# Kernel tuning notes

Measured on AMD Instinct MI355X. Metric: run time of the kernel, lower is better.

Reference implementation:

```python
import jax, jax.numpy as jnp
import numpy as np

EPS_NORM = 1e-5   # o_norm eps
EPS_L2 = 1e-6     # qk l2norm eps
CHUNK = 128       # chunk length for the scan


def _short_conv(x, w):
    # x: [B,T,C], w: [C,K]; causal depthwise conv followed by silu (ShortConvolution)
    K = w.shape[1]
    T = x.shape[1]
    xp = jnp.pad(x, ((0, 0), (K - 1, 0), (0, 0)))
    y = sum(xp[:, i:i + T, :] * w[:, i] for i in range(K))
    return jax.nn.silu(y)


def _l2norm(x):
    return x * jax.lax.rsqrt(jnp.sum(x * x, axis=-1, keepdims=True) + EPS_L2)


def _kda_scan(q, k, v, gk, beta):
    # gated delta rule: S_t = (I - b_t k_t k_t^T) diag(exp(gk_t)) S_{t-1} + b_t k_t v_t^T;  o_t = q_t^T S_t
    # q,k,gk: [B,T,H,Dk]; v: [B,T,H,Dv]; beta: [B,T,H]
    B, T, H, Dk = q.shape
    Dv = v.shape[-1]
    NC = T // CHUNK

    def c4(x):  # [B,T,H,D] -> [NC, CHUNK, B, H, D]
        return jnp.transpose(x.reshape(B, NC, CHUNK, H, x.shape[-1]), (1, 2, 0, 3, 4))

    qc, kc, vc, gc = c4(q), c4(k), c4(v), c4(gk)
    bc = jnp.transpose(beta.reshape(B, NC, CHUNK, H), (1, 2, 0, 3))

    def step(S, inp):  # S: [B,H,Dk,Dv]
        q_t, k_t, v_t, g_t, b_t = inp
        S = S * jnp.exp(g_t)[..., None]                       # per-key-channel decay
        err = v_t - jnp.einsum('bhk,bhkv->bhv', k_t, S)       # delta-rule error
        S = S + b_t[..., None, None] * (k_t[..., None] * err[..., None, :])
        o_t = jnp.einsum('bhk,bhkv->bhv', q_t, S)
        return S, o_t

    @jax.checkpoint
    def chunk_fn(S, xs):
        return jax.lax.scan(step, S, xs)

    S0 = jnp.zeros((B, H, Dk, Dv), q.dtype)
    _, o = jax.lax.scan(chunk_fn, S0, (qc, kc, vc, gc, bc))   # o: [NC, CHUNK, B, H, Dv]
    return jnp.transpose(o.reshape(T, B, H, Dv), (1, 0, 2, 3))


def _forward(hidden_states, q_w, k_w, v_w, q_conv_w, k_conv_w, v_conv_w,
             f_w1, f_w2, b_w, A_log, dt_bias, g_w1, g_w2, g_b2, o_norm_w, o_w):
    B, T, D = hidden_states.shape
    H = A_log.shape[0]
    Dv = o_norm_w.shape[0]
    Dk = q_w.shape[1] // H

    q = _short_conv(hidden_states @ q_w, q_conv_w).reshape(B, T, H, Dk)
    k = _short_conv(hidden_states @ k_w, k_conv_w).reshape(B, T, H, Dk)
    v = _short_conv(hidden_states @ v_w, v_conv_w).reshape(B, T, H, Dv)

    # fused_kda_gate: per-channel log-decay
    g = ((hidden_states @ f_w1) @ f_w2).reshape(B, T, H, Dk)
    gk = -jnp.exp(A_log)[:, None] * jax.nn.softplus(g + dt_bias.reshape(H, Dk))

    beta = jax.nn.sigmoid(hidden_states @ b_w)  # [B,T,H]

    q = _l2norm(q) * (Dk ** -0.5)
    k = _l2norm(k)

    o = _kda_scan(q, k, v, gk, beta)  # [B,T,H,Dv]

    # FusedRMSNormGated(activation='sigmoid')
    gate = ((hidden_states @ g_w1) @ g_w2 + g_b2).reshape(B, T, H, Dv)
    o = o * jax.lax.rsqrt(jnp.mean(o * o, axis=-1, keepdims=True) + EPS_NORM) * o_norm_w
    o = o * jax.nn.sigmoid(gate)

    return o.reshape(B, T, H * Dv) @ o_w


def setup_inputs() -> dict:
    key = jax.random.key(0)
    B, T, D = 2, 4096, 2048
    H, Dk, Dv = 16, 128, 128
    KD, VD = H * Dk, H * Dv
    Kc = 4
    ks = jax.random.split(key, 16)
    s = 0.02
    n = lambda kk, sh: jax.random.normal(kk, sh, jnp.float32) * s
    return dict(
        hidden_states=jax.random.normal(ks[0], (B, T, D), jnp.float32),
        q_w=n(ks[1], (D, KD)), k_w=n(ks[2], (D, KD)), v_w=n(ks[3], (D, VD)),
        q_conv_w=n(ks[4], (KD, Kc)), k_conv_w=n(ks[5], (KD, Kc)), v_conv_w=n(ks[6], (VD, Kc)),
        f_w1=n(ks[7], (D, Dv)), f_w2=n(ks[8], (Dv, KD)),
        b_w=n(ks[9], (D, H)),
        A_log=jnp.log(jax.random.uniform(ks[10], (H,), jnp.float32, 1.0, 16.0)),
        dt_bias=jnp.zeros((KD,), jnp.float32),
        g_w1=n(ks[11], (D, Dv)), g_w2=n(ks[12], (Dv, VD)), g_b2=jnp.zeros((VD,), jnp.float32),
        o_norm_w=jnp.ones((Dv,), jnp.float32),
        o_w=n(ks[13], (VD, D)),
    )


def reference(hidden_states, q_w, k_w, v_w, q_conv_w, k_conv_w, v_conv_w,
              f_w1, f_w2, b_w, A_log, dt_bias, g_w1, g_w2, g_b2, o_norm_w, o_w):
    return _forward(hidden_states, q_w, k_w, v_w, q_conv_w, k_conv_w, v_conv_w,
                    f_w1, f_w2, b_w, A_log, dt_bias, g_w1, g_w2, g_b2, o_norm_w, o_w)
```

## Files before the change

kernel.cpp:

```cpp
#include <hip/hip_runtime.h>
#include <math.h>


constexpr int NB = 2, NT = 4096, ND = 2048, NH = 16, DK = 128, DV = 128;
constexpr int MROWS = NB * NT;
constexpr int BHN   = NB * NH;
constexpr int CCH   = 16;
constexpr int NCH   = NT / CCH;

#define DEV static __device__ __forceinline__

typedef __attribute__((ext_vector_type(8))) short short8;
typedef __attribute__((ext_vector_type(4))) short short4v;
typedef __attribute__((ext_vector_type(4))) float f32x4;

DEV float sigmoidf_(float x) { return 1.0f / (1.0f + expf(-x)); }

DEV float bf2f(unsigned u) { return __uint_as_float(u << 16); }
DEV unsigned f2bf(float f) {
    unsigned u = __float_as_uint(f);
    return (u + 0x7fffu + ((u >> 16) & 1u)) >> 16;
}
DEV unsigned pack2(float a, float b) { return f2bf(a) | (f2bf(b) << 16); }

DEV void gl2lds16(const void* g, void* l) {
    __builtin_amdgcn_global_load_lds(
        (const __attribute__((address_space(1))) unsigned int*)g,
        (__attribute__((address_space(3))) unsigned int*)l, 16, 0, 0);
}
DEV void gl2lds4(const void* g, void* l) {
    __builtin_amdgcn_global_load_lds(
        (const __attribute__((address_space(1))) unsigned int*)g,
        (__attribute__((address_space(3))) unsigned int*)l, 4, 0, 0);
}

template <int CTRL>
DEV float dppadd(float x) {
    int y = __builtin_amdgcn_mov_dpp(__float_as_int(x), CTRL, 0xF, 0xF, true);
    return x + __int_as_float(y);
}
DEV float reduce16f(float x) {
    x = dppadd<0xB1>(x);
    x = dppadd<0x4E>(x);
    x = dppadd<0x141>(x);
    x = dppadd<0x140>(x);
    return x;
}

DEV float4 bflo(uint4 U) {
    return make_float4(bf2f(U.x & 0xffff), bf2f(U.x >> 16),
                       bf2f(U.y & 0xffff), bf2f(U.y >> 16));
}
DEV float4 bfhi(uint4 U) {
    return make_float4(bf2f(U.z & 0xffff), bf2f(U.z >> 16),
                       bf2f(U.w & 0xffff), bf2f(U.w >> 16));
}

DEV short4v lo4(short8 v) { short4v r; r[0]=v[0]; r[1]=v[1]; r[2]=v[2]; r[3]=v[3]; return r; }
DEV short4v hi4(short8 v) { short4v r; r[0]=v[4]; r[1]=v[5]; r[2]=v[6]; r[3]=v[7]; return r; }

DEV f32x4 mfma16(short4v a, short4v b, f32x4 c) {
#if __has_builtin(__builtin_amdgcn_mfma_f32_16x16x16bf16_1k)
    return __builtin_amdgcn_mfma_f32_16x16x16bf16_1k(a, b, c, 0, 0, 0);
#elif __has_builtin(__builtin_amdgcn_mfma_f32_16x16x16_bf16)
    return __builtin_amdgcn_mfma_f32_16x16x16_bf16(a, b, c, 0, 0, 0);
#else
    asm volatile("s_nop 1\n\t"
                 "v_mfma_f32_16x16x16_bf16 %0, %1, %2, %0\n\t"
                 "s_nop 7\n\t"
                 "s_nop 7"
                 : "+v"(c) : "v"(a), "v"(b));
    return c;
#endif
}

template <int OUTBF>
__global__ __launch_bounds__(256) void gemm_bf16(
    const unsigned short* __restrict__ A, const unsigned short* __restrict__ Bt,
    void* __restrict__ Cv, int Md, int Nd, int Kd)
{
    __shared__ unsigned short As[128 * 64];
    __shared__ unsigned short Bs[128 * 64];

    const int nbx = Nd >> 7;
    const int bx = blockIdx.x % nbx;
    const int by = blockIdx.x / nbx;
    const int m0 = by << 7, n0 = bx << 7;
    const int tid = threadIdx.x;
    const int lane = tid & 63, wid = tid >> 6;
    const int wr = wid >> 1, wc = wid & 1;

    const int srow  = tid >> 3;
    const int sslot = (tid & 7) ^ (srow & 7);
    const unsigned short* ag = A  + (size_t)(m0 + srow) * Kd + sslot * 8;
    const unsigned short* bg = Bt + (size_t)(n0 + srow) * Kd + sslot * 8;
    const size_t rstep32 = (size_t)32 * Kd;
    unsigned short* aw = As + wid * 512;
    unsigned short* bw = Bs + wid * 512;

    const int rrow  = lane & 15;
    const int khalf = lane >> 4;
    const int rswz  = rrow & 7;

    f32x4 zf = {0.f, 0.f, 0.f, 0.f};
    f32x4 acc[4][4];
#pragma unroll
    for (int m = 0; m < 4; m++)
#pragma unroll
        for (int n = 0; n < 4; n++) acc[m][n] = zf;

    for (int k0 = 0; k0 < Kd; k0 += 64) {
#pragma unroll
        for (int i = 0; i < 4; i++) {
            gl2lds16(ag + (size_t)i * rstep32 + k0, aw + i * 2048);
            gl2lds16(bg + (size_t)i * rstep32 + k0, bw + i * 2048);
        }
        __syncthreads();
#pragma unroll
        for (int kk = 0; kk < 2; kk++) {
            const int slot = (kk * 4 + khalf) ^ rswz;
            short8 a[4], b[4];
#pragma unroll
            for (int m = 0; m < 4; m++)
                a[m] = *(const short8*)&As[(wr * 64 + m * 16 + rrow) * 64 + slot * 8];
#pragma unroll
            for (int n = 0; n < 4; n++)
                b[n] = *(const short8*)&Bs[(wc * 64 + n * 16 + rrow) * 64 + slot * 8];
#pragma unroll
            for (int m = 0; m < 4; m++)
#pragma unroll
                for (int n = 0; n < 4; n++)
                    acc[m][n] = __builtin_amdgcn_mfma_f32_16x16x32_bf16(
                        a[m], b[n], acc[m][n], 0, 0, 0);
        }
        __syncthreads();
    }

#pragma unroll
    for (int m = 0; m < 4; m++) {
        const int rowb = m0 + wr * 64 + m * 16 + khalf * 4;
#pragma unroll
        for (int n = 0; n < 4; n++) {
            const int col = n0 + wc * 64 + n * 16 + rrow;
#pragma unroll
            for (int r = 0; r < 4; r++) {
                const float v = acc[m][n][r];
                if (OUTBF)
                    ((unsigned short*)Cv)[(size_t)(rowb + r) * Nd + col] =
                        (unsigned short)f2bf(v);
                else
                    ((float*)Cv)[(size_t)(rowb + r) * Nd + col] = v;
            }
        }
    }
}

__global__ __launch_bounds__(256) void wtrans(
    const float* __restrict__ W, unsigned short* __restrict__ Wt, int Kd, int Nd)
{
    __shared__ float T[64][65];
    const int nbk = Kd >> 6;
    const int bk = blockIdx.x % nbk, bn = blockIdx.x / nbk;
    const int k0 = bk << 6, n0 = bn << 6;
    const int tid = threadIdx.x;
    {
        const int r = tid >> 2, cg = tid & 3;
#pragma unroll
        for (int i = 0; i < 4; i++) {
            float4 f = *(const float4*)&W[(size_t)(k0 + r) * Nd + n0 + cg * 16 + i * 4];
            T[r][cg * 16 + i * 4 + 0] = f.x;
            T[r][cg * 16 + i * 4 + 1] = f.y;
            T[r][cg * 16 + i * 4 + 2] = f.z;
            T[r][cg * 16 + i * 4 + 3] = f.w;
        }
    }
    __syncthreads();
    {
        const int n = tid >> 2, kg = tid & 3;
#pragma unroll
        for (int i = 0; i < 2; i++) {
            unsigned o[4];
#pragma unroll
            for (int j = 0; j < 4; j++) {
                const int kk = kg * 16 + i * 8 + 2 * j;
                o[j] = pack2(T[kk][n], T[kk + 1][n]);
            }
            *(uint4*)&Wt[(size_t)(n0 + n) * Kd + k0 + kg * 16 + i * 8] =
                make_uint4(o[0], o[1], o[2], o[3]);
        }
    }
}

__global__ __launch_bounds__(256) void f2bf_k(
    const float* __restrict__ x, unsigned short* __restrict__ y, int n8)
{
    const int i = blockIdx.x * blockDim.x + threadIdx.x;
    if (i < n8) {
        float4 a = *(const float4*)&x[(size_t)i * 8];
        float4 b = *(const float4*)&x[(size_t)i * 8 + 4];
        uint4 o = make_uint4(pack2(a.x, a.y), pack2(a.z, a.w),
                             pack2(b.x, b.y), pack2(b.z, b.w));
        *(uint4*)&y[(size_t)i * 8] = o;
    }
}

template <int MODE>
__global__ __launch_bounds__(256) void conv_silu(
    const unsigned short* __restrict__ pre, const float* __restrict__ cw,
    unsigned short* __restrict__ outp)
{
    const int m = blockIdx.x;
    const int t = m & (NT - 1);
    const int b = m >> 12;
    const int tid = threadIdx.x;
    const int hd = tid * 8;
    const int h  = hd >> 7;
    const int d0 = hd & 127;

    float xr[4][8];
#pragma unroll
    for (int i = 0; i < 4; i++) {
        const int tt = t - 3 + i;
        if (tt >= 0) {
            uint4 u = *(const uint4*)(pre + (size_t)(m - 3 + i) * ND + hd);
            float4 lo = bflo(u), hi = bfhi(u);
            xr[i][0] = lo.x; xr[i][1] = lo.y; xr[i][2] = lo.z; xr[i][3] = lo.w;
            xr[i][4] = hi.x; xr[i][5] = hi.y; xr[i][6] = hi.z; xr[i][7] = hi.w;
        } else {
#pragma unroll
            for (int j = 0; j < 8; j++) xr[i][j] = 0.f;
        }
    }
    float y[8];
    float ssum = 0.f;
#pragma unroll
    for (int j = 0; j < 8; j++) {
        float4 w = *(const float4*)&cw[(size_t)(hd + j) * 4];
        float v = xr[0][j] * w.x + xr[1][j] * w.y + xr[2][j] * w.z + xr[3][j] * w.w;
        v = v * sigmoidf_(v);
        y[j] = v;
        ssum += v * v;
    }
    float scale = 1.f;
    if (MODE >= 1) {
        ssum = reduce16f(ssum);
        scale = rsqrtf(ssum + 1e-6f);
        if (MODE == 2) scale *= 0.08838834764831845f;
    }
    uint4 pk;
    pk.x = pack2(y[0] * scale, y[1] * scale);
    pk.y = pack2(y[2] * scale, y[3] * scale);
    pk.z = pack2(y[4] * scale, y[5] * scale);
    pk.w = pack2(y[6] * scale, y[7] * scale);
    unsigned short* dst = outp + ((size_t)(b * NH + h) * NT + t) * 128 + d0;
    *(uint4*)dst = pk;
}

__global__ __launch_bounds__(256) void gk_k(
    const unsigned short* __restrict__ g, const float* __restrict__ A_log,
    const float* __restrict__ dtb, _Float16* __restrict__ gko)
{
    const int m = blockIdx.x;
    const int t = m & (NT - 1);
    const int b = m >> 12;
    const int tid = threadIdx.x;
    const int hd = tid * 8, h = hd >> 7, d0 = hd & 127;
    const float ea = expf(A_log[h]);
    uint4 u = *(const uint4*)(g + (size_t)m * ND + hd);
    float4 lo = bflo(u), hi = bfhi(u);
    float4 b0 = *(const float4*)&dtb[hd], b1 = *(const float4*)&dtb[hd + 4];
    float xin[8] = {lo.x + b0.x, lo.y + b0.y, lo.z + b0.z, lo.w + b0.w,
                    hi.x + b1.x, hi.y + b1.y, hi.z + b1.z, hi.w + b1.w};
    union { _Float16 h8[8]; uint4 u4; } up;
#pragma unroll
    for (int j = 0; j < 8; j++) {
        float x = xin[j];
        float sp = (x > 20.f) ? x : log1pf(expf(x));
        up.h8[j] = (_Float16)(-ea * sp);
    }
    _Float16* dst = gko + ((size_t)(b * NH + h) * NT + t) * 128 + d0;
    *(uint4*)dst = up.u4;
}

__global__ __launch_bounds__(256) void beta_k(
    const float* __restrict__ hs, const float* __restrict__ bw,
    float* __restrict__ bt)
{
    __shared__ float sh[ND];
    __shared__ float part[16][17];
    const int m = blockIdx.x, tid = threadIdx.x;
    ((float4*)sh)[tid * 2]     = ((const float4*)(hs + (size_t)m * ND))[tid * 2];
    ((float4*)sh)[tid * 2 + 1] = ((const float4*)(hs + (size_t)m * ND))[tid * 2 + 1];
    __syncthreads();
    const int h = tid & 15, seg = tid >> 4;
    float p = 0.f;
#pragma unroll 8
    for (int j = 0; j < 128; j++)
        p += sh[seg * 128 + j] * bw[(size_t)(seg * 128 + j) * 16 + h];
    part[seg][h] = p;
    __syncthreads();
    if (tid < 16) {
        float s = 0.f;
#pragma unroll
        for (int i = 0; i < 16; i++) s += part[i][tid];
        const int t = m & (NT - 1), b = m >> 12;
        bt[(size_t)(b * NH + tid) * NT + t] = sigmoidf_(s);
    }
}

__global__ __launch_bounds__(256) void kda_prep(
    unsigned short* __restrict__ qn, unsigned short* __restrict__ kn,
    unsigned short* __restrict__ vv, unsigned short* __restrict__ gkh,
    const float* __restrict__ bt,
    float* __restrict__ BdB, float* __restrict__ eCB)
{
    __shared__ float cL[16][132];
    __shared__ float kL[16][132];
    __shared__ float qL[16][132];
    __shared__ float kapL[16][132];
    __shared__ float AbL[16][16];
    __shared__ float bL[16];
    __shared__ float sx[16][264];

    const int blk = blockIdx.x;
    const int bh  = blk >> 8;
    const int cc  = blk & 255;
    const int tid = threadIdx.x;
    const size_t ebase  = ((size_t)bh * NT + cc * 16) * 128;
    const size_t chbase = (size_t)bh * NCH + cc;

    if (tid < 16) bL[tid] = bt[(size_t)bh * NT + cc * 16 + tid];

    if (tid < 128) {
        const int d = tid;
        float c = 0.f;
#pragma unroll
        for (int i = 0; i < 16; i++) {
            float g = (float)(((const _Float16*)gkh)[ebase + i * 128 + d]);
            c += g;
            cL[i][d] = c;
            float kv = bf2f(kn[ebase + i * 128 + d]);
            float qv = bf2f(qn[ebase + i * 128 + d]);
            kL[i][d] = kv; qL[i][d] = qv;
            kapL[i][d] = kv * expf(c);
        }
        eCB[chbase * 128 + d] = expf(c);
    }
    __syncthreads();

    if (tid < 128) {
        const int d = tid;
        const int t = d >> 4, rr = d & 15;
        const int sw = (rr & 7) << 3;
        const float clast = cL[15][d];
        unsigned u[8];
#pragma unroll
        for (int e = 0; e < 8; e++) {
            float v0 = bL[2 * e]     * kL[2 * e][d]     * expf(clast - cL[2 * e][d]);
            float v1 = bL[2 * e + 1] * kL[2 * e + 1][d] * expf(clast - cL[2 * e + 1][d]);
            u[e] = pack2(v0, v1);
        }
        const unsigned bs = ((t >> 1) * 16 + rr) * 32 + (t & 1) * 4;
        unsigned short* base = gkh + chbase * 2048;
        *(uint2*)(base + ((bs +  0) ^ sw)) = make_uint2(u[0], u[1]);
        *(uint2*)(base + ((bs +  8) ^ sw)) = make_uint2(u[2], u[3]);
        *(uint2*)(base + ((bs + 16) ^ sw)) = make_uint2(u[4], u[5]);
        *(uint2*)(base + ((bs + 24) ^ sw)) = make_uint2(u[6], u[7]);
    }

    const int si = tid >> 4, sj = tid & 15;
    float aAcc = 0.f, bAcc = 0.f;
    if (si >= sj) {
        for (int d4 = 0; d4 < 128; d4 += 4) {
            float4 ci = *(const float4*)&cL[si][d4];
            float4 cj = *(const float4*)&cL[sj][d4];
            float4 ki = *(const float4*)&kL[si][d4];
            float4 kj = *(const float4*)&kL[sj][d4];
            float4 qi = *(const float4*)&qL[si][d4];
            float w;
            w = expf(ci.x - cj.x); aAcc += ki.x * kj.x * w; bAcc += qi.x * kj.x * w;
            w = expf(ci.y - cj.y); aAcc += ki.y * kj.y * w; bAcc += qi.y * kj.y * w;
            w = expf(ci.z - cj.z); aAcc += ki.z * kj.z * w; bAcc += qi.z * kj.z * w;
            w = expf(ci.w - cj.w); aAcc += ki.w * kj.w * w; bAcc += qi.w * kj.w * w;
        }
    }
    if (si > sj) AbL[si][sj] = aAcc * bL[sj];
    BdB[chbase * 256 + ((si * 16 + sj) ^ ((si & 7) << 2))] = bAcc * bL[sj];
    __syncthreads();

    {
        const int col = tid;
        float x[16];
#pragma unroll
        for (int i = 0; i < 16; i++)
            x[i] = (col < 128) ? kapL[i][col]
                               : bf2f(vv[ebase + (size_t)i * 128 + (col - 128)]);
#pragma unroll
        for (int i = 1; i < 16; i++) {
            float s = x[i];
#pragma unroll
            for (int l = 0; l < 15; l++)
                if (l < i) s -= AbL[i][l] * x[l];
            x[i] = s;
        }
#pragma unroll
        for (int i = 0; i < 16; i++) sx[i][col] = x[i];
    }
    __syncthreads();

    {
        const int row = tid >> 4, q16 = tid & 15;
        const int d0 = q16 * 8;
        const int t  = q16 >> 1;
        const int pos0 = (t >> 1) * 32 + (t & 1) * 4 + (q16 & 1) * 16;
        const int sw = (row & 7) << 3;
        const int oA = pos0 ^ sw;
        const int oB = (pos0 + 8) ^ sw;
        unsigned pu[4], qu[4];
#pragma unroll
        for (int e = 0; e < 4; e++) {
            pu[e] = pack2(-sx[row][d0 + 2 * e], -sx[row][d0 + 2 * e + 1]);
            qu[e] = pack2(qL[row][d0 + 2 * e]     * expf(cL[row][d0 + 2 * e]),
                          qL[row][d0 + 2 * e + 1] * expf(cL[row][d0 + 2 * e + 1]));
        }
        unsigned short* kb = kn + ebase + (size_t)row * 128;
        unsigned short* qb = qn + ebase + (size_t)row * 128;
        *(uint2*)(kb + oA) = make_uint2(pu[0], pu[1]);
        *(uint2*)(kb + oB) = make_uint2(pu[2], pu[3]);
        *(uint2*)(qb + oA) = make_uint2(qu[0], qu[1]);
        *(uint2*)(qb + oB) = make_uint2(qu[2], qu[3]);
    }
    if (tid < 128) {
        const int c = tid;
        unsigned u2[8];
#pragma unroll
        for (int e = 0; e < 8; e++)
            u2[e] = pack2(sx[2 * e][128 + c], sx[2 * e + 1][128 + c]);
        unsigned short* vb = vv + ebase + (size_t)c * 16;
        *(uint4*)(vb)     = make_uint4(u2[0], u2[1], u2[2], u2[3]);
        *(uint4*)(vb + 8) = make_uint4(u2[4], u2[5], u2[6], u2[7]);
    }
}

__global__ __launch_bounds__(64) void kda_scan4(
    const unsigned short* __restrict__ qn, const unsigned short* __restrict__ kn,
    const unsigned short* __restrict__ vv, const unsigned short* __restrict__ khat,
    const float* __restrict__ BdB, const float* __restrict__ eCB,
    float* __restrict__ osc)
{
    __shared__ unsigned short Pl[2][2048];
    __shared__ unsigned short Ql[2][2048];
    __shared__ unsigned short KHl[2][2048];
    __shared__ unsigned short Vl[2][256];
    __shared__ float eCl[2][128];
    __shared__ float Bdl[2][256];

    const int bh = blockIdx.x & 31;
    const int vg = blockIdx.x >> 5;
    const int lane = threadIdx.x;
    const int r16 = lane & 15, h4 = lane >> 4;
    const int bb = bh >> 4, hh = bh & 15;
    const int sw = (r16 & 7) << 3;

    f32x4 Sm[8];
    short4v Shi[8];
    const short4v z4 = {0, 0, 0, 0};
#pragma unroll
    for (int t = 0; t < 8; t++) { Sm[t] = (f32x4){0.f, 0.f, 0.f, 0.f}; Shi[t] = z4; }

    auto issue = [&](int cc, int buf) {
        const size_t ebase = ((size_t)bh * NT + cc * 16) * 128;
        const size_t chb = (size_t)bh * NCH + cc;
#pragma unroll
        for (int i = 0; i < 4; i++) {
            gl2lds16(kn + ebase + i * 512 + lane * 8, &Pl[buf][i * 512]);
            gl2lds16(qn + ebase + i * 512 + lane * 8, &Ql[buf][i * 512]);
            gl2lds16(khat + chb * 2048 + i * 512 + lane * 8, &KHl[buf][i * 512]);
        }
#pragma unroll
        for (int j = 0; j < 2; j++) {
            gl2lds4((const char*)(vv + ebase + (size_t)vg * 256) + j * 256 + lane * 4,
                    &Vl[buf][j * 128]);
            gl2lds4((const char*)(eCB + chb * 128) + j * 256 + lane * 4,
                    &eCl[buf][j * 64]);
        }
        gl2lds16((const char*)(BdB + chb * 256) + lane * 16, &Bdl[buf][0]);
    };

    issue(0, 0);
    for (int cc = 0; cc < NCH; ++cc) {
        const int cur = cc & 1;
        if (cc + 1 < NCH) {
            issue(cc + 1, cur ^ 1);
            asm volatile("s_waitcnt vmcnt(17)" ::: "memory");
        } else {
            asm volatile("s_waitcnt vmcnt(0)" ::: "memory");
        }
        __builtin_amdgcn_sched_barrier(0);

        const unsigned short* Pb  = &Pl[cur][0];
        const unsigned short* Qb  = &Ql[cur][0];
        const unsigned short* KHb = &KHl[cur][0];

        short8 Pp[4], Qp[4], KHp[4];
#pragma unroll
        for (int m = 0; m < 4; m++) {
            const int po = r16 * 128 + ((m * 32 + h4 * 8) ^ sw);
            Pp[m]  = *(const short8*)&Pb[po];
            Qp[m]  = *(const short8*)&Qb[po];
            KHp[m] = *(const short8*)&KHb[((m * 16 + r16) * 32 + h4 * 8) ^ sw];
        }
        short4v vvt = *(const short4v*)&Vl[cur][r16 * 16 + h4 * 4];
        float4 eCt[8];
#pragma unroll
        for (int t = 0; t < 8; t++)
            eCt[t] = *(const float4*)&eCl[cur][t * 16 + h4 * 4];
        float4 bd4 = *(const float4*)&Bdl[cur][(r16 * 16 + h4 * 4) ^ ((r16 & 7) << 2)];
        short4v bdf;
        bdf[0] = (short)f2bf(bd4.x); bdf[1] = (short)f2bf(bd4.y);
        bdf[2] = (short)f2bf(bd4.z); bdf[3] = (short)f2bf(bd4.w);

        f32x4 e0, e1 = {0.f, 0.f, 0.f, 0.f};
        f32x4 o0 = {0.f, 0.f, 0.f, 0.f}, o1 = {0.f, 0.f, 0.f, 0.f};
        e0[0] = bf2f((unsigned short)vvt[0]); e0[1] = bf2f((unsigned short)vvt[1]);
        e0[2] = bf2f((unsigned short)vvt[2]); e0[3] = bf2f((unsigned short)vvt[3]);
#pragma unroll
        for (int m = 0; m < 4; m++) {
            e0 = mfma16(lo4(Pp[m]), Shi[2 * m],     e0);
            e1 = mfma16(hi4(Pp[m]), Shi[2 * m + 1], e1);
            o0 = mfma16(lo4(Qp[m]), Shi[2 * m],     o0);
            o1 = mfma16(hi4(Qp[m]), Shi[2 * m + 1], o1);
        }
        f32x4 accE, accO;
        accE[0] = e0[0] + e1[0]; accE[1] = e0[1] + e1[1];
        accE[2] = e0[2] + e1[2]; accE[3] = e0[3] + e1[3];
        accO[0] = o0[0] + o1[0]; accO[1] = o0[1] + o1[1];
        accO[2] = o0[2] + o1[2]; accO[3] = o0[3] + o1[3];

        short4v ef;
        ef[0] = (short)f2bf(accE[0]); ef[1] = (short)f2bf(accE[1]);
        ef[2] = (short)f2bf(accE[2]); ef[3] = (short)f2bf(accE[3]);
        accO = mfma16(bdf, ef, accO);

#pragma unroll
        for (int t = 0; t < 8; t++) {
            const short4v khf = (t & 1) ? hi4(KHp[t >> 1]) : lo4(KHp[t >> 1]);
            f32x4 ns;
            ns[0] = eCt[t].x * Sm[t][0];
            ns[1] = eCt[t].y * Sm[t][1];
            ns[2] = eCt[t].z * Sm[t][2];
            ns[3] = eCt[t].w * Sm[t][3];
            ns = mfma16(khf, ef, ns);
            Sm[t] = ns;
            short4v nh;
            nh[0] = (short)f2bf(ns[0]); nh[1] = (short)f2bf(ns[1]);
            nh[2] = (short)f2bf(ns[2]); nh[3] = (short)f2bf(ns[3]);
            Shi[t] = nh;
        }

        const size_t obase = ((size_t)bb * NT + cc * 16) * ND + hh * 128 + vg * 16 + r16;
#pragma unroll
        for (int r = 0; r < 4; r++)
            osc[obase + (size_t)(h4 * 4 + r) * ND] = accO[r];
    }
}

__global__ __launch_bounds__(256) void gate_k(
    const float* __restrict__ osc, const unsigned short* __restrict__ gateb,
    const float* __restrict__ gb2, const float* __restrict__ onw,
    unsigned short* __restrict__ ogb)
{
    const int m = blockIdx.x, tid = threadIdx.x;
    const int hd = tid * 8, d0 = hd & 127;
    const float* op = osc + (size_t)m * ND + hd;
    float4 o0 = *(const float4*)op, o1 = *(const float4*)(op + 4);
    float ssum = o0.x * o0.x + o0.y * o0.y + o0.z * o0.z + o0.w * o0.w +
                 o1.x * o1.x + o1.y * o1.y + o1.z * o1.z + o1.w * o1.w;
    ssum = reduce16f(ssum);
    const float r = rsqrtf(ssum * (1.0f / 128.0f) + 1e-5f);
    uint4 gu = *(const uint4*)(gateb + (size_t)m * ND + hd);
    float4 gl = bflo(gu), gh = bfhi(gu);
    float4 b0 = *(const float4*)&gb2[hd], b1 = *(const float4*)&gb2[hd + 4];
    float4 w0 = *(const float4*)&onw[d0], w1 = *(const float4*)&onw[d0 + 4];
    float res[8];
    res[0] = o0.x * r * w0.x * sigmoidf_(gl.x + b0.x);
    res[1] = o0.y * r * w0.y * sigmoidf_(gl.y + b0.y);
    res[2] = o0.z * r * w0.z * sigmoidf_(gl.z + b0.z);
    res[3] = o0.w * r * w0.w * sigmoidf_(gl.w + b0.w);
    res[4] = o1.x * r * w1.x * sigmoidf_(gh.x + b1.x);
    res[5] = o1.y * r * w1.y * sigmoidf_(gh.y + b1.y);
    res[6] = o1.z * r * w1.z * sigmoidf_(gh.z + b1.z);
    res[7] = o1.w * r * w1.w * sigmoidf_(gh.w + b1.w);
    uint4 pk;
    pk.x = pack2(res[0], res[1]); pk.y = pack2(res[2], res[3]);
    pk.z = pack2(res[4], res[5]); pk.w = pack2(res[6], res[7]);
    *(uint4*)(ogb + (size_t)m * ND + hd) = pk;
}

__global__ void diag_fill(float* out, float val, int n) {
    for (int i = blockIdx.x * blockDim.x + threadIdx.x; i < n; i += gridDim.x * blockDim.x)
        out[i] = val;
}

extern "C" void kernel_launch(void* const* d_in, const int* in_sizes, int n_in,
                              void* d_out, int out_size, void* d_ws, size_t ws_size,
                              hipStream_t stream)
{
    const float* hs    = (const float*)d_in[0];
    const float* q_w   = (const float*)d_in[1];
    const float* k_w   = (const float*)d_in[2];
    const float* v_w   = (const float*)d_in[3];
    const float* qcw   = (const float*)d_in[4];
    const float* kcw   = (const float*)d_in[5];
    const float* vcw   = (const float*)d_in[6];
    const float* f_w1  = (const float*)d_in[7];
    const float* f_w2  = (const float*)d_in[8];
    const float* b_w   = (const float*)d_in[9];
    const float* A_log = (const float*)d_in[10];
    const float* dt_b  = (const float*)d_in[11];
    const float* g_w1  = (const float*)d_in[12];
    const float* g_w2  = (const float*)d_in[13];
    const float* g_b2  = (const float*)d_in[14];
    const float* onw   = (const float*)d_in[15];
    const float* o_w   = (const float*)d_in[16];
    float* out = (float*)d_out;

    const size_t SEQ = (size_t)BHN * NT;
    const size_t BF  = SEQ * 128 * 2;
    char* wsb = (char*)d_ws;
    size_t off = 0;
    unsigned short* qn   = (unsigned short*)(wsb + off); off += BF;
    unsigned short* kn   = (unsigned short*)(wsb + off); off += BF;
    unsigned short* vv   = (unsigned short*)(wsb + off); off += BF;
    unsigned short* dc   = (unsigned short*)(wsb + off); off += BF;
    unsigned short* P1   = (unsigned short*)(wsb + off); off += (size_t)MROWS * ND * 2;
    unsigned short* WT   = (unsigned short*)(wsb + off); off += (size_t)ND * ND * 2;
    unsigned short* fw1t = (unsigned short*)(wsb + off); off += (size_t)DK * ND * 2;
    unsigned short* fw2t = (unsigned short*)(wsb + off); off += (size_t)ND * DK * 2;
    unsigned short* gw1t = (unsigned short*)(wsb + off); off += (size_t)DK * ND * 2;
    unsigned short* gw2t = (unsigned short*)(wsb + off); off += (size_t)ND * DK * 2;
    unsigned short* f1b  = (unsigned short*)(wsb + off); off += (size_t)MROWS * DK * 2;
    unsigned short* g1b  = (unsigned short*)(wsb + off); off += (size_t)MROWS * DK * 2;
    float* bt  = (float*)(wsb + off); off += SEQ * 4;
    float* BdB = (float*)(wsb + off); off += (size_t)BHN * NCH * 256 * 4;
    float* eCB = (float*)(wsb + off); off += (size_t)BHN * NCH * 128 * 4;
    unsigned short* ogb = vv;
    unsigned short* hsb = (unsigned short*)d_out;

    if (ws_size < off) {
        diag_fill<<<512, 256, 0, stream>>>(out, 1.0e6f + (float)(ws_size >> 20), out_size);
        return;
    }

    dim3 blk(256);
    auto g2 = [](int Md, int Nd) { return dim3((unsigned)((Md >> 7) * (Nd >> 7))); };
    auto gt = [](int Kd, int Nd) { return dim3((unsigned)((Kd >> 6) * (Nd >> 6))); };

    f2bf_k<<<(MROWS * ND / 8 + 255) / 256, blk, 0, stream>>>(hs, hsb, MROWS * ND / 8);

    wtrans<<<gt(ND, ND), blk, 0, stream>>>(q_w, WT, ND, ND);
    gemm_bf16<1><<<g2(MROWS, ND), blk, 0, stream>>>(hsb, WT, P1, MROWS, ND, ND);
    conv_silu<2><<<MROWS, blk, 0, stream>>>(P1, qcw, qn);
    wtrans<<<gt(ND, ND), blk, 0, stream>>>(k_w, WT, ND, ND);
    gemm_bf16<1><<<g2(MROWS, ND), blk, 0, stream>>>(hsb, WT, P1, MROWS, ND, ND);
    conv_silu<1><<<MROWS, blk, 0, stream>>>(P1, kcw, kn);
    wtrans<<<gt(ND, ND), blk, 0, stream>>>(v_w, WT, ND, ND);
    gemm_bf16<1><<<g2(MROWS, ND), blk, 0, stream>>>(hsb, WT, P1, MROWS, ND, ND);
    conv_silu<0><<<MROWS, blk, 0, stream>>>(P1, vcw, vv);

    wtrans<<<gt(ND, DK), blk, 0, stream>>>(f_w1, fw1t, ND, DK);
    gemm_bf16<1><<<g2(MROWS, DK), blk, 0, stream>>>(hsb, fw1t, f1b, MROWS, DK, ND);
    wtrans<<<gt(DK, ND), blk, 0, stream>>>(f_w2, fw2t, DK, ND);
    gemm_bf16<1><<<g2(MROWS, ND), blk, 0, stream>>>(f1b, fw2t, P1, MROWS, ND, DK);
    gk_k<<<MROWS, blk, 0, stream>>>(P1, A_log, dt_b, (_Float16*)dc);

    wtrans<<<gt(ND, DK), blk, 0, stream>>>(g_w1, gw1t, ND, DK);
    gemm_bf16<1><<<g2(MROWS, DK), blk, 0, stream>>>(hsb, gw1t, g1b, MROWS, DK, ND);
    wtrans<<<gt(DK, ND), blk, 0, stream>>>(g_w2, gw2t, DK, ND);
    gemm_bf16<1><<<g2(MROWS, ND), blk, 0, stream>>>(g1b, gw2t, P1, MROWS, ND, DK);

    beta_k<<<MROWS, blk, 0, stream>>>(hs, b_w, bt);

    kda_prep<<<BHN * NCH, blk, 0, stream>>>(qn, kn, vv, dc, bt, BdB, eCB);
    kda_scan4<<<BHN * 8, 64, 0, stream>>>(qn, kn, vv, dc, BdB, eCB, out);

    gate_k<<<MROWS, blk, 0, stream>>>(out, P1, g_b2, onw, ogb);

    wtrans<<<gt(ND, ND), blk, 0, stream>>>(o_w, WT, ND, ND);
    gemm_bf16<0><<<g2(MROWS, ND), blk, 0, stream>>>(ogb, WT, out, MROWS, ND, ND);
}
```

Measured before the change: 1.216 ms.

## Triple-buffer scan prefetch, split MFMA accumulator chains, swizzle GEMM block order

The scan kernel moves from double to triple buffering in LDS, prefetching two chunks ahead with adjusted vmcnt waits, so global load latency is hidden behind more compute. The dependent MFMA chains for the error and output projections are split into four accumulators each, shortening the serial dependency per chunk. The GEMM remaps block indices in groups of eight, likely to cluster neighbouring tiles per XCD for better L2 reuse. Costs are more LDS per block and hand-tuned wait counts that must match the exact number of issued loads.

```diff
diff --git a/kernel.cpp b/kernel.cpp
--- a/kernel.cpp
+++ b/kernel.cpp
@@ -83,8 +83,14 @@
     __shared__ unsigned short Bs[128 * 64];
 
     const int nbx = Nd >> 7;
-    const int bx = blockIdx.x % nbx;
-    const int by = blockIdx.x / nbx;
+    unsigned blk = blockIdx.x;
+    const unsigned nwg = gridDim.x;
+    if ((nwg & 7u) == 0u) {
+        const unsigned cpx = nwg >> 3;
+        blk = (blk & 7u) * cpx + (blk >> 3);
+    }
+    const int bx = blk % nbx;
+    const int by = blk / nbx;
     const int m0 = by << 7, n0 = bx << 7;
     const int tid = threadIdx.x;
     const int lane = tid & 63, wid = tid >> 6;
@@ -442,18 +448,18 @@
     }
 }
 
-__global__ __launch_bounds__(64) void kda_scan4(
+__global__ __launch_bounds__(64) void kda_scan5(
     const unsigned short* __restrict__ qn, const unsigned short* __restrict__ kn,
     const unsigned short* __restrict__ vv, const unsigned short* __restrict__ khat,
     const float* __restrict__ BdB, const float* __restrict__ eCB,
     float* __restrict__ osc)
 {
-    __shared__ unsigned short Pl[2][2048];
-    __shared__ unsigned short Ql[2][2048];
-    __shared__ unsigned short KHl[2][2048];
-    __shared__ unsigned short Vl[2][256];
-    __shared__ float eCl[2][128];
-    __shared__ float Bdl[2][256];
+    __shared__ unsigned short Pl[3][2048];
+    __shared__ unsigned short Ql[3][2048];
+    __shared__ unsigned short KHl[3][2048];
+    __shared__ unsigned short Vl[3][256];
+    __shared__ float eCl[3][128];
+    __shared__ float Bdl[3][256];
 
     const int bh = blockIdx.x & 31;
     const int vg = blockIdx.x >> 5;
@@ -488,13 +494,19 @@
     };
 
     issue(0, 0);
+    issue(1, 1);
+    int cur = 0;
     for (int cc = 0; cc < NCH; ++cc) {
-        const int cur = cc & 1;
-        if (cc + 1 < NCH) {
-            issue(cc + 1, cur ^ 1);
-            asm volatile("s_waitcnt vmcnt(17)" ::: "memory");
+        if (cc + 2 < NCH) {
+            int nb = cur + 2; if (nb >= 3) nb -= 3;
+            issue(cc + 2, nb);
+        }
+        if (cc < 2) {
+            asm volatile("s_waitcnt vmcnt(34)" ::: "memory");
+        } else if (cc + 2 < NCH) {
+            asm volatile("s_waitcnt vmcnt(42)" ::: "memory");
         } else {
-            asm volatile("s_waitcnt vmcnt(0)" ::: "memory");
+            asm volatile("s_waitcnt vmcnt(8)" ::: "memory");
         }
         __builtin_amdgcn_sched_barrier(0);
 
@@ -520,22 +532,35 @@
         bdf[0] = (short)f2bf(bd4.x); bdf[1] = (short)f2bf(bd4.y);
         bdf[2] = (short)f2bf(bd4.z); bdf[3] = (short)f2bf(bd4.w);
 
-        f32x4 e0, e1 = {0.f, 0.f, 0.f, 0.f};
-        f32x4 o0 = {0.f, 0.f, 0.f, 0.f}, o1 = {0.f, 0.f, 0.f, 0.f};
+        const f32x4 zf = {0.f, 0.f, 0.f, 0.f};
+        f32x4 e0, e1 = zf, e2 = zf, e3 = zf;
+        f32x4 o0 = zf, o1 = zf, o2 = zf, o3 = zf;
         e0[0] = bf2f((unsigned short)vvt[0]); e0[1] = bf2f((unsigned short)vvt[1]);
         e0[2] = bf2f((unsigned short)vvt[2]); e0[3] = bf2f((unsigned short)vvt[3]);
-#pragma unroll
-        for (int m = 0; m < 4; m++) {
-            e0 = mfma16(lo4(Pp[m]), Shi[2 * m],     e0);
-            e1 = mfma16(hi4(Pp[m]), Shi[2 * m + 1], e1);
-            o0 = mfma16(lo4(Qp[m]), Shi[2 * m],     o0);
-            o1 = mfma16(hi4(Qp[m]), Shi[2 * m + 1], o1);
-        }
+
+        e0 = mfma16(lo4(Pp[0]), Shi[0], e0);
+        e1 = mfma16(hi4(Pp[0]), Shi[1], e1);
+        o0 = mfma16(lo4(Qp[0]), Shi[0], o0);
+        o1 = mfma16(hi4(Qp[0]), Shi[1], o1);
+        e2 = mfma16(lo4(Pp[1]), Shi[2], e2);
+        e3 = mfma16(hi4(Pp[1]), Shi[3], e3);
+        o2 = mfma16(lo4(Qp[1]), Shi[2], o2);
+        o3 = mfma16(hi4(Qp[1]), Shi[3], o3);
+        e0 = mfma16(lo4(Pp[2]), Shi[4], e0);
+        e1 = mfma16(hi4(Pp[2]), Shi[5], e1);
+        o0 = mfma16(lo4(Qp[2]), Shi[4], o0);
+        o1 = mfma16(hi4(Qp[2]), Shi[5], o1);
+        e2 = mfma16(lo4(Pp[3]), Shi[6], e2);
+        e3 = mfma16(hi4(Pp[3]), Shi[7], e3);
+        o2 = mfma16(lo4(Qp[3]), Shi[6], o2);
+        o3 = mfma16(hi4(Qp[3]), Shi[7], o3);
+
         f32x4 accE, accO;
-        accE[0] = e0[0] + e1[0]; accE[1] = e0[1] + e1[1];
-        accE[2] = e0[2] + e1[2]; accE[3] = e0[3] + e1[3];
-        accO[0] = o0[0] + o1[0]; accO[1] = o0[1] + o1[1];
-        accO[2] = o0[2] + o1[2]; accO[3] = o0[3] + o1[3];
+#pragma unroll
+        for (int r = 0; r < 4; r++) {
+            accE[r] = (e0[r] + e1[r]) + (e2[r] + e3[r]);
+            accO[r] = (o0[r] + o1[r]) + (o2[r] + o3[r]);
+        }
 
         short4v ef;
         ef[0] = (short)f2bf(accE[0]); ef[1] = (short)f2bf(accE[1]);
@@ -562,6 +587,8 @@
 #pragma unroll
         for (int r = 0; r < 4; r++)
             osc[obase + (size_t)(h4 * 4 + r) * ND] = accO[r];
+
+        cur = cur + 1; if (cur >= 3) cur = 0;
     }
 }
 
@@ -682,7 +709,7 @@
     beta_k<<<MROWS, blk, 0, stream>>>(hs, b_w, bt);
 
     kda_prep<<<BHN * NCH, blk, 0, stream>>>(qn, kn, vv, dc, bt, BdB, eCB);
-    kda_scan4<<<BHN * 8, 64, 0, stream>>>(qn, kn, vv, dc, BdB, eCB, out);
+    kda_scan5<<<BHN * 8, 64, 0, stream>>>(qn, kn, vv, dc, BdB, eCB, out);
 
     gate_k<<<MROWS, blk, 0, stream>>>(out, P1, g_b2, onw, ogb);
 
```

Measured after the change: 1.246 ms. 1.02x slower.
